# Kernel optimization log

Hardware: AMD Instinct MI355X
Metric: run time of the kernel (lower is better)

The kernel has to match this reference:

```python
import jax, jax.numpy as jnp
import numpy as np

NUM_LABELS = 512
NUM_DEMOG = 4
N = 65536
D = 512


def setup_inputs() -> dict:
    key = jax.random.key(0)
    k1, k2, k3 = jax.random.split(key, 3)
    feats = jax.random.normal(k1, (N, D), dtype=jnp.float32)
    labels = jax.random.randint(k2, (N,), 0, NUM_LABELS, dtype=jnp.int64)
    demog_labels = jax.random.randint(k3, (N,), 0, NUM_DEMOG, dtype=jnp.int64)
    return {"feats": feats, "labels": labels, "demog_labels": demog_labels}


def reference(feats, labels, demog_labels):
    # Group id = (demog, label) pair -> flat segment id.
    G = NUM_DEMOG * NUM_LABELS
    seg = (demog_labels * NUM_LABELS + labels).astype(jnp.int32)  # [N]

    ones = jnp.ones((feats.shape[0],), dtype=feats.dtype)
    cnt = jax.ops.segment_sum(ones, seg, num_segments=G)          # [G]
    sums = jax.ops.segment_sum(feats, seg, num_segments=G)        # [G, D]
    safe_cnt = jnp.maximum(cnt, 1.0)
    mu = sums / safe_cnt[:, None]                                 # per-group mean

    # Per-sample squared distance to its group mean (== diagonal of the
    # centered Gram matrix in the original, without the O(n^2) matmul).
    d = feats - mu[seg]                                           # [N, D]
    sq = jnp.sum(d * d, axis=1)                                   # [N]

    grp_mean_dist = jax.ops.segment_sum(sq, seg, num_segments=G) / safe_cnt  # [G]

    present = (cnt > 0).astype(feats.dtype).reshape(NUM_DEMOG, NUM_LABELS)
    gm = grp_mean_dist.reshape(NUM_DEMOG, NUM_LABELS)
    # Mean over present (demog, subject) groups within each demog.
    intra = jnp.sum(gm * present, axis=1) / jnp.maximum(jnp.sum(present, axis=1), 1.0)  # [NUM_DEMOG]

    mu_intra = jnp.mean(intra)
    loss = jnp.mean(jnp.abs(intra - mu_intra))
    return loss
```

## Files before the change

kernel.cpp:

```cpp
#include <hip/hip_runtime.h>
#include <hip/hip_bf16.h>

#define NN 65536
#define DD 512
#define NUM_LABELS 512
#define NUM_DEMOG 4
#define GG (NUM_DEMOG * NUM_LABELS)
#define CAP 128

__global__ void k_hist(const int* __restrict__ labels,
                       const int* __restrict__ demog,
                       int* __restrict__ cnt,
                       int* __restrict__ order) {
    int i = blockIdx.x * blockDim.x + threadIdx.x;
    if (i >= NN) return;
    int seg = demog[i] * NUM_LABELS + labels[i];
    int pos = atomicAdd(&cnt[seg], 1);
    if (pos < CAP) order[seg * CAP + pos] = i;
}

__device__ __forceinline__ void gather16(const float4* __restrict__ fv,
                                         const int* sidx, int jstart, int c,
                                         int col, float4& acc, float& ssq) {
    float4 v[16];
    float  w[16];
#pragma unroll
    for (int k = 0; k < 16; ++k) {
        int j = jstart + 2 * k;
        v[k] = fv[(size_t)sidx[j] * (DD / 4) + col];
        w[k] = (j < c) ? 1.f : 0.f;
    }
#pragma unroll
    for (int k = 0; k < 16; ++k) {
        acc.x += w[k] * v[k].x;
        acc.y += w[k] * v[k].y;
        acc.z += w[k] * v[k].z;
        acc.w += w[k] * v[k].w;
        ssq += w[k] * (v[k].x * v[k].x + v[k].y * v[k].y +
                       v[k].z * v[k].z + v[k].w * v[k].w);
    }
}

__global__ __launch_bounds__(256)
void k_group(const float* __restrict__ feats,
             const int* __restrict__ cnt,
             const int* __restrict__ order,
             float* __restrict__ gmArr) {
    int g = blockIdx.x;
    int t = threadIdx.x;
    int col = t & 127;
    int rp  = t >> 7;

    __shared__ int sidx[CAP];
    int oi = (t < CAP) ? order[g * CAP + t] : 0;
    int c = cnt[g];
    if (c > CAP) c = CAP;
    if (t < CAP) sidx[t] = (t < c) ? oi : 0;
    __syncthreads();

    const float4* fv = (const float4*)feats;
    float4 acc = make_float4(0.f, 0.f, 0.f, 0.f);
    float ssq = 0.f;

    gather16(fv, sidx, rp, c, col, acc, ssq);
    if (c > 32) {
        gather16(fv, sidx, rp + 32, c, col, acc, ssq);
        for (int j = rp + 64; j < c; j += 2) {
            float4 v = fv[(size_t)sidx[j] * (DD / 4) + col];
            acc.x += v.x; acc.y += v.y; acc.z += v.z; acc.w += v.w;
            ssq += v.x * v.x + v.y * v.y + v.z * v.z + v.w * v.w;
        }
    }

    __shared__ float4 accbuf[128];
    if (rp == 1) accbuf[col] = acc;
    __syncthreads();
    float n2p = 0.f;
    if (rp == 0) {
        float4 o = accbuf[col];
        float x = acc.x + o.x, y = acc.y + o.y, z = acc.z + o.z, w = acc.w + o.w;
        n2p = x * x + y * y + z * z + w * w;
    }

    for (int off = 32; off > 0; off >>= 1) {
        ssq += __shfl_down(ssq, off);
        n2p += __shfl_down(n2p, off);
    }
    __shared__ float red[8];
    if ((t & 63) == 0) {
        int wid = t >> 6;
        red[wid * 2]     = ssq;
        red[wid * 2 + 1] = n2p;
    }
    __syncthreads();
    if (t == 0) {
        float gm = 0.f;
        if (c > 0) {
            float S  = red[0] + red[2] + red[4] + red[6];
            float N2 = red[1] + red[3] + red[5] + red[7];
            gm = (S - N2 / (float)c) / (float)c;
        }
        gmArr[g] = gm;
    }
}

__global__ __launch_bounds__(256)
void k_final(const int* __restrict__ cnt,
             const float* __restrict__ gmArr,
             float* __restrict__ out) {
    int t = threadIdx.x;
    __shared__ float sred[8];
    __shared__ float intra[NUM_DEMOG];

    for (int d = 0; d < NUM_DEMOG; ++d) {
        float s = 0.f;
        float p = 0.f;
        for (int l = t; l < NUM_LABELS; l += 256) {
            int g = d * NUM_LABELS + l;
            if (cnt[g] > 0) { s += gmArr[g]; p += 1.f; }
        }
        for (int off = 32; off > 0; off >>= 1) {
            s += __shfl_down(s, off);
            p += __shfl_down(p, off);
        }
        if ((t & 63) == 0) {
            int wid = t >> 6;
            sred[wid * 2]     = s;
            sred[wid * 2 + 1] = p;
        }
        __syncthreads();
        if (t == 0) {
            float S = sred[0] + sred[2] + sred[4] + sred[6];
            float P = sred[1] + sred[3] + sred[5] + sred[7];
            intra[d] = S / fmaxf(P, 1.f);
        }
        __syncthreads();
    }
    if (t == 0) {
        float m = 0.f;
        for (int d = 0; d < NUM_DEMOG; ++d) m += intra[d];
        m *= (1.f / NUM_DEMOG);
        float l = 0.f;
        for (int d = 0; d < NUM_DEMOG; ++d) l += fabsf(intra[d] - m);
        out[0] = l * (1.f / NUM_DEMOG);
    }
}

extern "C" void kernel_launch(void* const* d_in, const int* in_sizes, int n_in,
                              void* d_out, int out_size, void* d_ws, size_t ws_size,
                              hipStream_t stream) {
    const float* feats = (const float*)d_in[0];
    const int* labels  = (const int*)d_in[1];
    const int* demog   = (const int*)d_in[2];
    float* out = (float*)d_out;

    int*   cnt   = (int*)d_ws;
    float* gmArr = (float*)(cnt + GG);
    int*   order = (int*)(gmArr + GG);

    hipMemsetAsync(d_ws, 0, GG * sizeof(int), stream);

    k_hist<<<NN / 256, 256, 0, stream>>>(labels, demog, cnt, order);
    k_group<<<GG, 256, 0, stream>>>(feats, cnt, order, gmArr);
    k_final<<<1, 256, 0, stream>>>(cnt, gmArr, out);
}
```

Before: 213.8 us.

## Split each group's column range across four blocks with per-slice partial sums

Each group is now handled by four blocks, each covering a 32-float4 column slice, with eight rows gathered in parallel per block instead of two. Each block writes a partial S - N2/c value, and the final kernel sums the four partials and divides by the count. This raises the number of blocks and the memory-level parallelism per group, aiming to hide gather latency. In exchange it reloads the index list once per slice and launches more small blocks.

```diff
diff --git a/kernel.cpp b/kernel.cpp
--- a/kernel.cpp
+++ b/kernel.cpp
@@ -7,6 +7,7 @@
 #define NUM_DEMOG 4
 #define GG (NUM_DEMOG * NUM_LABELS)
 #define CAP 128
+#define NSLICE 4
 
 __global__ void k_hist(const int* __restrict__ labels,
                        const int* __restrict__ demog,
@@ -19,37 +20,16 @@
     if (pos < CAP) order[seg * CAP + pos] = i;
 }
 
-__device__ __forceinline__ void gather16(const float4* __restrict__ fv,
-                                         const int* sidx, int jstart, int c,
-                                         int col, float4& acc, float& ssq) {
-    float4 v[16];
-    float  w[16];
-#pragma unroll
-    for (int k = 0; k < 16; ++k) {
-        int j = jstart + 2 * k;
-        v[k] = fv[(size_t)sidx[j] * (DD / 4) + col];
-        w[k] = (j < c) ? 1.f : 0.f;
-    }
-#pragma unroll
-    for (int k = 0; k < 16; ++k) {
-        acc.x += w[k] * v[k].x;
-        acc.y += w[k] * v[k].y;
-        acc.z += w[k] * v[k].z;
-        acc.w += w[k] * v[k].w;
-        ssq += w[k] * (v[k].x * v[k].x + v[k].y * v[k].y +
-                       v[k].z * v[k].z + v[k].w * v[k].w);
-    }
-}
-
 __global__ __launch_bounds__(256)
 void k_group(const float* __restrict__ feats,
              const int* __restrict__ cnt,
              const int* __restrict__ order,
-             float* __restrict__ gmArr) {
-    int g = blockIdx.x;
-    int t = threadIdx.x;
-    int col = t & 127;
-    int rp  = t >> 7;
+             float* __restrict__ part) {
+    int g     = blockIdx.x >> 2;
+    int slice = blockIdx.x & 3;
+    int t     = threadIdx.x;
+    int tcol  = t & 31;
+    int rp    = t >> 5;
 
     __shared__ int sidx[CAP];
     int oi = (t < CAP) ? order[g * CAP + t] : 0;
@@ -59,27 +39,49 @@
     __syncthreads();
 
     const float4* fv = (const float4*)feats;
+    int fcol = slice * 32 + tcol;
+
     float4 acc = make_float4(0.f, 0.f, 0.f, 0.f);
     float ssq = 0.f;
 
-    gather16(fv, sidx, rp, c, col, acc, ssq);
-    if (c > 32) {
-        gather16(fv, sidx, rp + 32, c, col, acc, ssq);
-        for (int j = rp + 64; j < c; j += 2) {
-            float4 v = fv[(size_t)sidx[j] * (DD / 4) + col];
-            acc.x += v.x; acc.y += v.y; acc.z += v.z; acc.w += v.w;
-            ssq += v.x * v.x + v.y * v.y + v.z * v.z + v.w * v.w;
+    {
+        float4 v[8];
+        float  w[8];
+#pragma unroll
+        for (int k = 0; k < 8; ++k) {
+            int j = rp + 8 * k;
+            v[k] = fv[(size_t)sidx[j] * (DD / 4) + fcol];
+            w[k] = (j < c) ? 1.f : 0.f;
+        }
+#pragma unroll
+        for (int k = 0; k < 8; ++k) {
+            acc.x += w[k] * v[k].x;
+            acc.y += w[k] * v[k].y;
+            acc.z += w[k] * v[k].z;
+            acc.w += w[k] * v[k].w;
+            ssq += w[k] * (v[k].x * v[k].x + v[k].y * v[k].y +
+                           v[k].z * v[k].z + v[k].w * v[k].w);
         }
     }
+    for (int j = 64 + rp; j < c; j += 8) {
+        float4 v = fv[(size_t)sidx[j] * (DD / 4) + fcol];
+        acc.x += v.x; acc.y += v.y; acc.z += v.z; acc.w += v.w;
+        ssq += v.x * v.x + v.y * v.y + v.z * v.z + v.w * v.w;
+    }
 
-    __shared__ float4 accbuf[128];
-    if (rp == 1) accbuf[col] = acc;
+    __shared__ float4 accbuf[8][32];
+    accbuf[rp][tcol] = acc;
     __syncthreads();
+
     float n2p = 0.f;
     if (rp == 0) {
-        float4 o = accbuf[col];
-        float x = acc.x + o.x, y = acc.y + o.y, z = acc.z + o.z, w = acc.w + o.w;
-        n2p = x * x + y * y + z * z + w * w;
+        float4 s = accbuf[0][tcol];
+#pragma unroll
+        for (int k = 1; k < 8; ++k) {
+            float4 o = accbuf[k][tcol];
+            s.x += o.x; s.y += o.y; s.z += o.z; s.w += o.w;
+        }
+        n2p = s.x * s.x + s.y * s.y + s.z * s.z + s.w * s.w;
     }
 
     for (int off = 32; off > 0; off >>= 1) {
@@ -94,19 +96,19 @@
     }
     __syncthreads();
     if (t == 0) {
-        float gm = 0.f;
+        float val = 0.f;
         if (c > 0) {
             float S  = red[0] + red[2] + red[4] + red[6];
             float N2 = red[1] + red[3] + red[5] + red[7];
-            gm = (S - N2 / (float)c) / (float)c;
+            val = S - N2 / (float)c;
         }
-        gmArr[g] = gm;
+        part[blockIdx.x] = val;
     }
 }
 
 __global__ __launch_bounds__(256)
 void k_final(const int* __restrict__ cnt,
-             const float* __restrict__ gmArr,
+             const float* __restrict__ part,
              float* __restrict__ out) {
     int t = threadIdx.x;
     __shared__ float sred[8];
@@ -117,7 +119,13 @@
         float p = 0.f;
         for (int l = t; l < NUM_LABELS; l += 256) {
             int g = d * NUM_LABELS + l;
-            if (cnt[g] > 0) { s += gmArr[g]; p += 1.f; }
+            int c = cnt[g];
+            if (c > 0) {
+                float q = part[4 * g] + part[4 * g + 1] +
+                          part[4 * g + 2] + part[4 * g + 3];
+                s += q / (float)c;
+                p += 1.f;
+            }
         }
         for (int off = 32; off > 0; off >>= 1) {
             s += __shfl_down(s, off);
@@ -155,12 +163,12 @@
     float* out = (float*)d_out;
 
     int*   cnt   = (int*)d_ws;
-    float* gmArr = (float*)(cnt + GG);
-    int*   order = (int*)(gmArr + GG);
+    float* part  = (float*)(cnt + GG);
+    int*   order = (int*)(part + GG * NSLICE);
 
     hipMemsetAsync(d_ws, 0, GG * sizeof(int), stream);
 
     k_hist<<<NN / 256, 256, 0, stream>>>(labels, demog, cnt, order);
-    k_group<<<GG, 256, 0, stream>>>(feats, cnt, order, gmArr);
-    k_final<<<1, 256, 0, stream>>>(cnt, gmArr, out);
+    k_group<<<GG * NSLICE, 256, 0, stream>>>(feats, cnt, order, part);
+    k_final<<<1, 256, 0, stream>>>(cnt, part, out);
 }
```

Result: no change. 213.7 us (-0.0%).
